# Optimization experiments

Measured on AMD Instinct MI355X. Metric: run time of the kernel, lower is better.

Reference implementation:

```python
import jax, jax.numpy as jnp
import numpy as np

B, K, D = 16384, 512, 256

def setup_inputs() -> dict:
    key = jax.random.key(0)
    kz, kc = jax.random.split(key)
    z = jax.random.normal(kz, (B, D), dtype=jnp.float32)
    # matches nn.Parameter(torch.randn(n_codes, d_dim) * 0.1)
    codebook = jax.random.normal(kc, (K, D), dtype=jnp.float32) * 0.1
    return {"z": z, "codebook": codebook}

def reference(z, codebook):
    """Eval-mode forward of SFDiVeQ: project each z onto the nearest line
    segment between consecutive codewords. Vectorizes the original Python
    loop over K-1 segments via GEMMs; returns (z_q, indices, lambdas, dists).
    """
    c_i = codebook[:-1]                    # (K-1, D) segment starts
    seg = codebook[1:] - c_i               # (K-1, D) segment vectors
    seg_len_sq = jnp.sum(seg * seg, axis=-1) + 1e-8        # (K-1,)

    # t = ((z - c_i) . seg) / |seg|^2, clamped to [0, 1]
    dot = z @ seg.T - jnp.sum(c_i * seg, axis=-1)          # (B, K-1) = (z - c_i).seg
    t = jnp.clip(dot / seg_len_sq, 0.0, 1.0)               # (B, K-1)

    # |z - c_i|^2 via expansion (avoids (B, K-1, D) intermediate)
    zz = jnp.sum(z * z, axis=-1, keepdims=True)            # (B, 1)
    cc = jnp.sum(c_i * c_i, axis=-1)                       # (K-1,)
    zc = z @ c_i.T                                         # (B, K-1)
    d0 = zz - 2.0 * zc + cc                                # (B, K-1)

    # |z - (c_i + t*seg)|^2 = |z - c_i|^2 - 2 t (z - c_i).seg + t^2 |seg|^2
    dist_sq = jnp.maximum(d0 - 2.0 * t * dot + t * t * seg_len_sq, 0.0)
    dists_all = jnp.sqrt(dist_sq)                          # (B, K-1)

    # running-min with strict '<' keeps first minimum -> argmin (first tie) matches
    idx = jnp.argmin(dists_all, axis=-1)                   # (B,) int
    rows = jnp.arange(z.shape[0])
    t_best = t[rows, idx]                                  # (B,) lambdas
    best_point = c_i[idx] + t_best[:, None] * seg[idx]     # (B, D) nearest = z_q (eval)
    dists = dists_all[rows, idx]                           # (B,)
    return best_point, idx, t_best, dists
```

## Files before the change

### kernel.cpp

```cpp
#include <hip/hip_runtime.h>
#include <math.h>

#define B_ROWS 16384
#define K_CB   512
#define D_DIM  256
#define NSEG   511
#define BM     64
#define NGROUPS 5
#define SEGS_PER_GROUP 126

__global__ __launch_bounds__(64) void seg_consts_kernel(const float* __restrict__ cb,
                                                        float* __restrict__ sls,
                                                        float* __restrict__ cs,
                                                        float* __restrict__ cc) {
    int j = blockIdx.x;
    int lane = threadIdx.x;
    const float4* a4 = reinterpret_cast<const float4*>(cb + (size_t)j * D_DIM);
    const float4* b4 = reinterpret_cast<const float4*>(cb + (size_t)(j + 1) * D_DIM);
    float4 a = a4[lane];
    float4 b = b4[lane];
    float sx = b.x - a.x, sy = b.y - a.y, sz = b.z - a.z, sw = b.w - a.w;
    float p_sls = sx*sx + sy*sy + sz*sz + sw*sw;
    float p_cs  = a.x*sx + a.y*sy + a.z*sz + a.w*sw;
    float p_cc  = a.x*a.x + a.y*a.y + a.z*a.z + a.w*a.w;
    #pragma unroll
    for (int m = 32; m >= 1; m >>= 1) {
        p_sls += __shfl_xor(p_sls, m, 64);
        p_cs  += __shfl_xor(p_cs,  m, 64);
        p_cc  += __shfl_xor(p_cc,  m, 64);
    }
    if (lane == 0) {
        sls[j] = p_sls + 1e-8f;
        cs[j]  = p_cs;
        cc[j]  = p_cc;
    }
}

__global__ __launch_bounds__(256) void main_kernel(const float* __restrict__ z,
                                                   const float* __restrict__ cb,
                                                   const float* __restrict__ sls_g,
                                                   const float* __restrict__ cs_g,
                                                   const float* __restrict__ cc_g,
                                                   float4* __restrict__ cand) {
    __shared__ __align__(16) float zs[64][68];
    __shared__ __align__(16) float csh[64][68];
    __shared__ float W[64][65];
    __shared__ float zzs[64];
    __shared__ float bd2s[64];
    __shared__ float bts[64];
    __shared__ int   bidxs[64];

    int t = threadIdx.x;
    int row0 = blockIdx.x * BM;
    int seg_base = blockIdx.y * SEGS_PER_GROUP;
    int tr = t >> 4;
    int tc = t & 15;

    {
        int r = t >> 2, q = t & 3;
        const float4* zp = reinterpret_cast<const float4*>(z + (size_t)(row0 + r) * D_DIM + q * 64);
        float s = 0.f;
        #pragma unroll
        for (int i = 0; i < 16; ++i) {
            float4 v = zp[i];
            s += v.x*v.x + v.y*v.y + v.z*v.z + v.w*v.w;
        }
        s += __shfl_xor(s, 1, 64);
        s += __shfl_xor(s, 2, 64);
        if (q == 0) zzs[r] = s;
    }
    if (t < 64) { bd2s[t] = INFINITY; bidxs[t] = 0x7fffffff; bts[t] = 0.f; }
    __syncthreads();

    for (int ch = 0; ch < 2; ++ch) {
        int col0 = seg_base + ch * 63;
        if (col0 > NSEG - 1) break;

        float acc[4][4];
        #pragma unroll
        for (int r = 0; r < 4; ++r)
            #pragma unroll
            for (int c = 0; c < 4; ++c) acc[r][c] = 0.f;

        for (int dk = 0; dk < 4; ++dk) {
            int d0 = dk * 64;
            #pragma unroll
            for (int i = 0; i < 4; ++i) {
                int f  = i * 256 + t;
                int r  = f >> 4;
                int dq = f & 15;
                float4 v = *reinterpret_cast<const float4*>(z + (size_t)(row0 + r) * D_DIM + d0 + dq * 4);
                *reinterpret_cast<float4*>(&zs[r][dq * 4]) = v;
                int gc = col0 + r;
                float4 w;
                if (gc < K_CB) w = *reinterpret_cast<const float4*>(cb + (size_t)gc * D_DIM + d0 + dq * 4);
                else           w = make_float4(0.f, 0.f, 0.f, 0.f);
                *reinterpret_cast<float4*>(&csh[r][dq * 4]) = w;
            }
            __syncthreads();
            #pragma unroll
            for (int d4 = 0; d4 < 16; ++d4) {
                float4 za[4], cv[4];
                #pragma unroll
                for (int r = 0; r < 4; ++r) za[r] = *reinterpret_cast<const float4*>(&zs[tr + 16 * r][d4 * 4]);
                #pragma unroll
                for (int c = 0; c < 4; ++c) cv[c] = *reinterpret_cast<const float4*>(&csh[tc + 16 * c][d4 * 4]);
                #pragma unroll
                for (int r = 0; r < 4; ++r)
                    #pragma unroll
                    for (int c = 0; c < 4; ++c) {
                        acc[r][c] += za[r].x * cv[c].x;
                        acc[r][c] += za[r].y * cv[c].y;
                        acc[r][c] += za[r].z * cv[c].z;
                        acc[r][c] += za[r].w * cv[c].w;
                    }
            }
            __syncthreads();
        }

        #pragma unroll
        for (int r = 0; r < 4; ++r)
            #pragma unroll
            for (int c = 0; c < 4; ++c)
                W[tr + 16 * r][tc + 16 * c] = acc[r][c];
        __syncthreads();

        int seg_hi = min(col0 + 62, NSEG - 1);
        #pragma unroll
        for (int r = 0; r < 4; ++r) {
            int row = tr + 16 * r;
            float zzr = zzs[row];
            float bd = INFINITY; int bj = 0x7fffffff; float btt = 0.f;
            #pragma unroll
            for (int c = 0; c < 4; ++c) {
                int jl = tc + 16 * c;
                int j  = col0 + jl;
                if (jl < 63 && j <= seg_hi) {
                    float w0 = W[row][jl];
                    float w1 = W[row][jl + 1];
                    float slsj = sls_g[j], csj = cs_g[j], ccj = cc_g[j];
                    float dot = w1 - w0 - csj;
                    float tt = dot / slsj;
                    tt = fminf(fmaxf(tt, 0.f), 1.f);
                    float d2 = zzr - 2.f * w0 + ccj - 2.f * tt * dot + tt * tt * slsj;
                    d2 = fmaxf(d2, 0.f);
                    if (d2 < bd) { bd = d2; bj = j; btt = tt; }
                }
            }
            #pragma unroll
            for (int m = 8; m >= 1; m >>= 1) {
                float od = __shfl_xor(bd, m, 64);
                int   oj = __shfl_xor(bj, m, 64);
                float ot = __shfl_xor(btt, m, 64);
                if (od < bd || (od == bd && oj < bj)) { bd = od; bj = oj; btt = ot; }
            }
            if (tc == 0) {
                if (bd < bd2s[row] || (bd == bd2s[row] && bj < bidxs[row])) {
                    bd2s[row] = bd; bidxs[row] = bj; bts[row] = btt;
                }
            }
        }
        __syncthreads();
    }

    if (t < 64) {
        cand[(size_t)blockIdx.y * B_ROWS + row0 + t] =
            make_float4(bd2s[t], bts[t], (float)bidxs[t], 0.f);
    }
}

__global__ __launch_bounds__(256) void combine_kernel(const float4* __restrict__ cand,
                                                      const float* __restrict__ cb,
                                                      float* __restrict__ out) {
    float* out_bp  = out;
    float* out_idx = out + (size_t)B_ROWS * D_DIM;
    float* out_t   = out_idx + B_ROWS;
    float* out_d   = out_t + B_ROWS;

    __shared__ float4 sel[4];
    int t = threadIdx.x;
    int rloc = t >> 6, lane = t & 63;
    int row = blockIdx.x * 4 + rloc;

    if (lane == 0) {
        float bd = INFINITY; float bt = 0.f; int bj = 0x7fffffff;
        #pragma unroll
        for (int g = 0; g < NGROUPS; ++g) {
            float4 cg = cand[(size_t)g * B_ROWS + row];
            int j = (int)cg.z;
            if (cg.x < bd || (cg.x == bd && j < bj)) { bd = cg.x; bt = cg.y; bj = j; }
        }
        sel[rloc] = make_float4(bd, bt, (float)bj, 0.f);
    }
    __syncthreads();

    float4 s = sel[rloc];
    int j = (int)s.z;
    float tt = s.y;
    const float4* c0 = reinterpret_cast<const float4*>(cb + (size_t)j * D_DIM);
    const float4* c1 = reinterpret_cast<const float4*>(cb + (size_t)(j + 1) * D_DIM);
    float4 a = c0[lane], b = c1[lane];
    float4 bp = make_float4(a.x + tt * (b.x - a.x),
                            a.y + tt * (b.y - a.y),
                            a.z + tt * (b.z - a.z),
                            a.w + tt * (b.w - a.w));
    reinterpret_cast<float4*>(out_bp + (size_t)row * D_DIM)[lane] = bp;
    if (lane == 0) {
        out_idx[row] = s.z;
        out_t[row]   = tt;
        out_d[row]   = sqrtf(s.x);
    }
}

extern "C" void kernel_launch(void* const* d_in, const int* in_sizes, int n_in,
                              void* d_out, int out_size, void* d_ws, size_t ws_size,
                              hipStream_t stream) {
    const float* z  = (const float*)d_in[0];
    const float* cb = (const float*)d_in[1];
    float* ws  = (float*)d_ws;
    float* sls = ws;
    float* cs  = ws + 512;
    float* cc  = ws + 1024;
    float4* cand = (float4*)(ws + 1536);
    float* out = (float*)d_out;

    seg_consts_kernel<<<NSEG, 64, 0, stream>>>(cb, sls, cs, cc);
    main_kernel<<<dim3(B_ROWS / BM, NGROUPS), 256, 0, stream>>>(z, cb, sls, cs, cc, cand);
    combine_kernel<<<B_ROWS / 4, 256, 0, stream>>>(cand, cb, out);
}
```

Before: 169.5 us.

## Restructure segment-distance GEMM into 128x128 tiles with shuffle-based neighbor access

Measured after the change: 163.5 us. 3.5% less time.

```diff
diff --git a/kernel.cpp b/kernel.cpp
--- a/kernel.cpp
+++ b/kernel.cpp
@@ -5,210 +5,205 @@
 #define K_CB   512
 #define D_DIM  256
 #define NSEG   511
-#define BM     64
-#define NGROUPS 5
-#define SEGS_PER_GROUP 126
-
-__global__ __launch_bounds__(64) void seg_consts_kernel(const float* __restrict__ cb,
-                                                        float* __restrict__ sls,
-                                                        float* __restrict__ cs,
-                                                        float* __restrict__ cc) {
-    int j = blockIdx.x;
-    int lane = threadIdx.x;
-    const float4* a4 = reinterpret_cast<const float4*>(cb + (size_t)j * D_DIM);
-    const float4* b4 = reinterpret_cast<const float4*>(cb + (size_t)(j + 1) * D_DIM);
-    float4 a = a4[lane];
-    float4 b = b4[lane];
-    float sx = b.x - a.x, sy = b.y - a.y, sz = b.z - a.z, sw = b.w - a.w;
-    float p_sls = sx*sx + sy*sy + sz*sz + sw*sw;
-    float p_cs  = a.x*sx + a.y*sy + a.z*sz + a.w*sw;
-    float p_cc  = a.x*a.x + a.y*a.y + a.z*a.z + a.w*a.w;
-    #pragma unroll
-    for (int m = 32; m >= 1; m >>= 1) {
-        p_sls += __shfl_xor(p_sls, m, 64);
-        p_cs  += __shfl_xor(p_cs,  m, 64);
-        p_cc  += __shfl_xor(p_cc,  m, 64);
-    }
-    if (lane == 0) {
-        sls[j] = p_sls + 1e-8f;
-        cs[j]  = p_cs;
-        cc[j]  = p_cc;
-    }
-}
-
-__global__ __launch_bounds__(256) void main_kernel(const float* __restrict__ z,
-                                                   const float* __restrict__ cb,
-                                                   const float* __restrict__ sls_g,
-                                                   const float* __restrict__ cs_g,
-                                                   const float* __restrict__ cc_g,
-                                                   float4* __restrict__ cand) {
-    __shared__ __align__(16) float zs[64][68];
-    __shared__ __align__(16) float csh[64][68];
-    __shared__ float W[64][65];
-    __shared__ float zzs[64];
-    __shared__ float bd2s[64];
-    __shared__ float bts[64];
-    __shared__ int   bidxs[64];
-
+#define NG     4
+
+#define WS_WBND 1536
+#define WS_ZZ   50688
+#define WS_CAND 67072
+
+__global__ __launch_bounds__(256) void prologue_kernel(const float* __restrict__ z,
+                                                       const float* __restrict__ cb,
+                                                       float* __restrict__ sls,
+                                                       float* __restrict__ cs,
+                                                       float* __restrict__ cc,
+                                                       float* __restrict__ wbnd,
+                                                       float* __restrict__ zz) {
+    int bid = blockIdx.x;
     int t = threadIdx.x;
-    int row0 = blockIdx.x * BM;
-    int seg_base = blockIdx.y * SEGS_PER_GROUP;
+    int lane = t & 63;
+    if (bid < 128) {
+        int j = bid * 4 + (t >> 6);
+        if (j == NSEG) {
+            if (lane == 0) { sls[NSEG] = 1e30f; cs[NSEG] = 0.f; cc[NSEG] = 0.f; }
+            return;
+        }
+        float4 a = reinterpret_cast<const float4*>(cb + (size_t)j * D_DIM)[lane];
+        float4 b = reinterpret_cast<const float4*>(cb + (size_t)(j + 1) * D_DIM)[lane];
+        float sx = b.x - a.x, sy = b.y - a.y, sz = b.z - a.z, sw = b.w - a.w;
+        float p0 = sx*sx + sy*sy + sz*sz + sw*sw;
+        float p1 = a.x*sx + a.y*sy + a.z*sz + a.w*sw;
+        float p2 = a.x*a.x + a.y*a.y + a.z*a.z + a.w*a.w;
+        #pragma unroll
+        for (int m = 32; m >= 1; m >>= 1) {
+            p0 += __shfl_xor(p0, m);
+            p1 += __shfl_xor(p1, m);
+            p2 += __shfl_xor(p2, m);
+        }
+        if (lane == 0) { sls[j] = p0 + 1e-8f; cs[j] = p1; cc[j] = p2; }
+    } else {
+        int row = (bid - 128) * 4 + (t >> 6);
+        float4 zv = reinterpret_cast<const float4*>(z + (size_t)row * D_DIM)[lane];
+        float pz = zv.x*zv.x + zv.y*zv.y + zv.z*zv.z + zv.w*zv.w;
+        #pragma unroll
+        for (int m = 32; m >= 1; m >>= 1) pz += __shfl_xor(pz, m);
+        if (lane == 0) zz[row] = pz;
+        #pragma unroll
+        for (int gi = 0; gi < 3; ++gi) {
+            int col = 128 * (gi + 1);
+            float4 cv = reinterpret_cast<const float4*>(cb + (size_t)col * D_DIM)[lane];
+            float p = zv.x*cv.x + zv.y*cv.y + zv.z*cv.z + zv.w*cv.w;
+            #pragma unroll
+            for (int m = 32; m >= 1; m >>= 1) p += __shfl_xor(p, m);
+            if (lane == 0) wbnd[(size_t)gi * B_ROWS + row] = p;
+        }
+    }
+}
+
+__global__ __launch_bounds__(256, 2) void main_kernel(const float* __restrict__ z,
+                                                      const float* __restrict__ cb,
+                                                      const float* __restrict__ sls_g,
+                                                      const float* __restrict__ cs_g,
+                                                      const float* __restrict__ cc_g,
+                                                      const float* __restrict__ wbnd,
+                                                      float4* __restrict__ cand) {
+    __shared__ __align__(16) float zs[128][36];
+    __shared__ __align__(16) float csh[128][36];
+    __shared__ float sl_s[128], cs_s[128], cc_s[128];
+
+    int t = threadIdx.x;
+    int row0 = blockIdx.x * 128;
+    int g = blockIdx.y;
+    int col0 = g * 128;
     int tr = t >> 4;
     int tc = t & 15;
-
-    {
-        int r = t >> 2, q = t & 3;
-        const float4* zp = reinterpret_cast<const float4*>(z + (size_t)(row0 + r) * D_DIM + q * 64);
-        float s = 0.f;
-        #pragma unroll
-        for (int i = 0; i < 16; ++i) {
-            float4 v = zp[i];
-            s += v.x*v.x + v.y*v.y + v.z*v.z + v.w*v.w;
-        }
-        s += __shfl_xor(s, 1, 64);
-        s += __shfl_xor(s, 2, 64);
-        if (q == 0) zzs[r] = s;
-    }
-    if (t < 64) { bd2s[t] = INFINITY; bidxs[t] = 0x7fffffff; bts[t] = 0.f; }
-    __syncthreads();
-
-    for (int ch = 0; ch < 2; ++ch) {
-        int col0 = seg_base + ch * 63;
-        if (col0 > NSEG - 1) break;
-
-        float acc[4][4];
-        #pragma unroll
-        for (int r = 0; r < 4; ++r)
+    int l = t & 63;
+
+    if (t < 128) {
+        sl_s[t] = sls_g[col0 + t];
+        cs_s[t] = cs_g[col0 + t];
+        cc_s[t] = cc_g[col0 + t];
+    }
+
+    float acc[8][8];
+    #pragma unroll
+    for (int r = 0; r < 8; ++r)
+        #pragma unroll
+        for (int c = 0; c < 8; ++c) acc[r][c] = 0.f;
+
+    for (int kc = 0; kc < 8; ++kc) {
+        int d0 = kc * 32;
+        __syncthreads();
+        #pragma unroll
+        for (int i = 0; i < 4; ++i) {
+            int f = i * 256 + t;
+            int r = f >> 3;
+            int kq = f & 7;
+            float4 v = *reinterpret_cast<const float4*>(z + (size_t)(row0 + r) * D_DIM + d0 + kq * 4);
+            *reinterpret_cast<float4*>(&zs[r][kq * 4]) = v;
+            float4 w = *reinterpret_cast<const float4*>(cb + (size_t)(col0 + r) * D_DIM + d0 + kq * 4);
+            *reinterpret_cast<float4*>(&csh[r][kq * 4]) = w;
+        }
+        __syncthreads();
+        #pragma unroll
+        for (int k4 = 0; k4 < 8; ++k4) {
+            float4 za[8];
             #pragma unroll
-            for (int c = 0; c < 4; ++c) acc[r][c] = 0.f;
-
-        for (int dk = 0; dk < 4; ++dk) {
-            int d0 = dk * 64;
+            for (int r = 0; r < 8; ++r)
+                za[r] = *reinterpret_cast<const float4*>(&zs[tr + 16 * r][k4 * 4]);
             #pragma unroll
-            for (int i = 0; i < 4; ++i) {
-                int f  = i * 256 + t;
-                int r  = f >> 4;
-                int dq = f & 15;
-                float4 v = *reinterpret_cast<const float4*>(z + (size_t)(row0 + r) * D_DIM + d0 + dq * 4);
-                *reinterpret_cast<float4*>(&zs[r][dq * 4]) = v;
-                int gc = col0 + r;
-                float4 w;
-                if (gc < K_CB) w = *reinterpret_cast<const float4*>(cb + (size_t)gc * D_DIM + d0 + dq * 4);
-                else           w = make_float4(0.f, 0.f, 0.f, 0.f);
-                *reinterpret_cast<float4*>(&csh[r][dq * 4]) = w;
-            }
-            __syncthreads();
-            #pragma unroll
-            for (int d4 = 0; d4 < 16; ++d4) {
-                float4 za[4], cv[4];
+            for (int c = 0; c < 8; ++c) {
+                float4 cv = *reinterpret_cast<const float4*>(&csh[tc + 16 * c][k4 * 4]);
                 #pragma unroll
-                for (int r = 0; r < 4; ++r) za[r] = *reinterpret_cast<const float4*>(&zs[tr + 16 * r][d4 * 4]);
-                #pragma unroll
-                for (int c = 0; c < 4; ++c) cv[c] = *reinterpret_cast<const float4*>(&csh[tc + 16 * c][d4 * 4]);
-                #pragma unroll
-                for (int r = 0; r < 4; ++r)
-                    #pragma unroll
-                    for (int c = 0; c < 4; ++c) {
-                        acc[r][c] += za[r].x * cv[c].x;
-                        acc[r][c] += za[r].y * cv[c].y;
-                        acc[r][c] += za[r].z * cv[c].z;
-                        acc[r][c] += za[r].w * cv[c].w;
-                    }
-            }
-            __syncthreads();
-        }
-
-        #pragma unroll
-        for (int r = 0; r < 4; ++r)
-            #pragma unroll
-            for (int c = 0; c < 4; ++c)
-                W[tr + 16 * r][tc + 16 * c] = acc[r][c];
-        __syncthreads();
-
-        int seg_hi = min(col0 + 62, NSEG - 1);
-        #pragma unroll
-        for (int r = 0; r < 4; ++r) {
-            int row = tr + 16 * r;
-            float zzr = zzs[row];
-            float bd = INFINITY; int bj = 0x7fffffff; float btt = 0.f;
-            #pragma unroll
-            for (int c = 0; c < 4; ++c) {
-                int jl = tc + 16 * c;
-                int j  = col0 + jl;
-                if (jl < 63 && j <= seg_hi) {
-                    float w0 = W[row][jl];
-                    float w1 = W[row][jl + 1];
-                    float slsj = sls_g[j], csj = cs_g[j], ccj = cc_g[j];
-                    float dot = w1 - w0 - csj;
-                    float tt = dot / slsj;
-                    tt = fminf(fmaxf(tt, 0.f), 1.f);
-                    float d2 = zzr - 2.f * w0 + ccj - 2.f * tt * dot + tt * tt * slsj;
-                    d2 = fmaxf(d2, 0.f);
-                    if (d2 < bd) { bd = d2; bj = j; btt = tt; }
+                for (int r = 0; r < 8; ++r) {
+                    acc[r][c] += za[r].x * cv.x;
+                    acc[r][c] += za[r].y * cv.y;
+                    acc[r][c] += za[r].z * cv.z;
+                    acc[r][c] += za[r].w * cv.w;
                 }
             }
-            #pragma unroll
-            for (int m = 8; m >= 1; m >>= 1) {
-                float od = __shfl_xor(bd, m, 64);
-                int   oj = __shfl_xor(bj, m, 64);
-                float ot = __shfl_xor(btt, m, 64);
-                if (od < bd || (od == bd && oj < bj)) { bd = od; bj = oj; btt = ot; }
-            }
-            if (tc == 0) {
-                if (bd < bd2s[row] || (bd == bd2s[row] && bj < bidxs[row])) {
-                    bd2s[row] = bd; bidxs[row] = bj; bts[row] = btt;
-                }
-            }
-        }
-        __syncthreads();
-    }
-
-    if (t < 64) {
-        cand[(size_t)blockIdx.y * B_ROWS + row0 + t] =
-            make_float4(bd2s[t], bts[t], (float)bidxs[t], 0.f);
+        }
+    }
+
+    float wbv[8];
+    #pragma unroll
+    for (int r = 0; r < 8; ++r) wbv[r] = 0.f;
+    if (g < 3 && tc == 15) {
+        #pragma unroll
+        for (int r = 0; r < 8; ++r)
+            wbv[r] = wbnd[(size_t)g * B_ROWS + row0 + tr + 16 * r];
+    }
+
+    #pragma unroll
+    for (int r = 0; r < 8; ++r) {
+        int row = tr + 16 * r;
+        float firstw[8];
+        #pragma unroll
+        for (int c = 1; c < 8; ++c) firstw[c] = __shfl(acc[r][c], l & 48);
+        float bd = 1e38f; int bj = 0x3fffffff; float bt = 0.f;
+        #pragma unroll
+        for (int c = 0; c < 8; ++c) {
+            float w0 = acc[r][c];
+            float shA = __shfl(w0, l + 1);
+            float w1 = (tc == 15) ? ((c < 7) ? firstw[c + 1] : wbv[r]) : shA;
+            int jl = tc + 16 * c;
+            int j = col0 + jl;
+            float slsj = sl_s[jl], csj = cs_s[jl], ccj = cc_s[jl];
+            float dot = w1 - w0 - csj;
+            float tt = fminf(fmaxf(dot / slsj, 0.f), 1.f);
+            float d2 = ccj - 2.f * w0 + tt * (tt * slsj - 2.f * dot);
+            if (j < NSEG && d2 < bd) { bd = d2; bj = j; bt = tt; }
+        }
+        #pragma unroll
+        for (int m = 1; m <= 8; m <<= 1) {
+            float od = __shfl_xor(bd, m);
+            int   oj = __shfl_xor(bj, m);
+            float ot = __shfl_xor(bt, m);
+            if (od < bd || (od == bd && oj < bj)) { bd = od; bj = oj; bt = ot; }
+        }
+        if (tc == 0)
+            cand[(size_t)(row0 + row) * NG + g] = make_float4(bd, bt, (float)bj, 0.f);
     }
 }
 
 __global__ __launch_bounds__(256) void combine_kernel(const float4* __restrict__ cand,
                                                       const float* __restrict__ cb,
+                                                      const float* __restrict__ zz,
                                                       float* __restrict__ out) {
     float* out_bp  = out;
     float* out_idx = out + (size_t)B_ROWS * D_DIM;
     float* out_t   = out_idx + B_ROWS;
     float* out_d   = out_t + B_ROWS;
 
-    __shared__ float4 sel[4];
+    __shared__ float sj[256];
+    __shared__ float st[256];
+
     int t = threadIdx.x;
-    int rloc = t >> 6, lane = t & 63;
-    int row = blockIdx.x * 4 + rloc;
-
-    if (lane == 0) {
-        float bd = INFINITY; float bt = 0.f; int bj = 0x7fffffff;
-        #pragma unroll
-        for (int g = 0; g < NGROUPS; ++g) {
-            float4 cg = cand[(size_t)g * B_ROWS + row];
-            int j = (int)cg.z;
-            if (cg.x < bd || (cg.x == bd && j < bj)) { bd = cg.x; bt = cg.y; bj = j; }
-        }
-        sel[rloc] = make_float4(bd, bt, (float)bj, 0.f);
-    }
+    int row = blockIdx.x * 256 + t;
+    const float4* cp = cand + (size_t)row * NG;
+    float4 c0 = cp[0], c1 = cp[1], c2 = cp[2], c3 = cp[3];
+    float bd = c0.x, bt = c0.y, bj = c0.z;
+    if (c1.x < bd) { bd = c1.x; bt = c1.y; bj = c1.z; }
+    if (c2.x < bd) { bd = c2.x; bt = c2.y; bj = c2.z; }
+    if (c3.x < bd) { bd = c3.x; bt = c3.y; bj = c3.z; }
+    sj[t] = bj; st[t] = bt;
+    out_idx[row] = bj;
+    out_t[row]   = bt;
+    out_d[row]   = sqrtf(fmaxf(bd + zz[row], 0.f));
     __syncthreads();
 
-    float4 s = sel[rloc];
-    int j = (int)s.z;
-    float tt = s.y;
-    const float4* c0 = reinterpret_cast<const float4*>(cb + (size_t)j * D_DIM);
-    const float4* c1 = reinterpret_cast<const float4*>(cb + (size_t)(j + 1) * D_DIM);
-    float4 a = c0[lane], b = c1[lane];
-    float4 bp = make_float4(a.x + tt * (b.x - a.x),
-                            a.y + tt * (b.y - a.y),
-                            a.z + tt * (b.z - a.z),
-                            a.w + tt * (b.w - a.w));
-    reinterpret_cast<float4*>(out_bp + (size_t)row * D_DIM)[lane] = bp;
-    if (lane == 0) {
-        out_idx[row] = s.z;
-        out_t[row]   = tt;
-        out_d[row]   = sqrtf(s.x);
+    int lane = t & 63, sub = t >> 6;
+    #pragma unroll 4
+    for (int it = 0; it < 64; ++it) {
+        int rl = it * 4 + sub;
+        int j = (int)sj[rl];
+        float tt = st[rl];
+        float4 a = reinterpret_cast<const float4*>(cb + (size_t)j * D_DIM)[lane];
+        float4 b = reinterpret_cast<const float4*>(cb + (size_t)(j + 1) * D_DIM)[lane];
+        float4 bp = make_float4(a.x + tt * (b.x - a.x),
+                                a.y + tt * (b.y - a.y),
+                                a.z + tt * (b.z - a.z),
+                                a.w + tt * (b.w - a.w));
+        reinterpret_cast<float4*>(out_bp + (size_t)(blockIdx.x * 256 + rl) * D_DIM)[lane] = bp;
     }
 }
 
@@ -218,13 +213,15 @@
     const float* z  = (const float*)d_in[0];
     const float* cb = (const float*)d_in[1];
     float* ws  = (float*)d_ws;
-    float* sls = ws;
-    float* cs  = ws + 512;
-    float* cc  = ws + 1024;
-    float4* cand = (float4*)(ws + 1536);
+    float* sls  = ws;
+    float* cs   = ws + 512;
+    float* cc   = ws + 1024;
+    float* wbnd = ws + WS_WBND;
+    float* zz   = ws + WS_ZZ;
+    float4* cand = (float4*)(ws + WS_CAND);
     float* out = (float*)d_out;
 
-    seg_consts_kernel<<<NSEG, 64, 0, stream>>>(cb, sls, cs, cc);
-    main_kernel<<<dim3(B_ROWS / BM, NGROUPS), 256, 0, stream>>>(z, cb, sls, cs, cc, cand);
-    combine_kernel<<<B_ROWS / 4, 256, 0, stream>>>(cand, cb, out);
-}
+    prologue_kernel<<<128 + B_ROWS / 4, 256, 0, stream>>>(z, cb, sls, cs, cc, wbnd, zz);
+    main_kernel<<<dim3(B_ROWS / 128, NG), 256, 0, stream>>>(z, cb, sls, cs, cc, wbnd, cand);
+    combine_kernel<<<B_ROWS / 256, 256, 0, stream>>>(cand, cb, zz, out);
+}
```
